# Performance work log

Hardware: AMD Instinct MI355X
Metric: run time of the kernel (lower is better)

The kernel has to match this reference:

```python
import jax, jax.numpy as jnp
import numpy as np

SA_LAMBDA = 1.0
IC_LAMBDA = 1.0
EPS = 1e-12  # torch F.normalize eps


def setup_inputs() -> dict:
    key = jax.random.key(0)
    k1, k2, k3, k4 = jax.random.split(key, 4)
    TF = jax.random.normal(k1, (16, 512, 32, 32), dtype=jnp.float32)
    SF = jax.random.normal(k2, (16, 512, 32, 32), dtype=jnp.float32)
    t_out = jax.random.normal(k3, (16, 21, 128, 128), dtype=jnp.float32)
    s_out = jax.random.normal(k4, (16, 21, 128, 128), dtype=jnp.float32)
    return {"TF": TF, "SF": SF, "t_out": t_out, "s_out": s_out}


def _l2_normalize_last(A):
    # matches torch.nn.functional.normalize(x, dim=2): x / max(||x||, eps)
    n = jnp.linalg.norm(A, axis=-1, keepdims=True)
    return A / jnp.maximum(n, EPS)


def _channel_weighted_spatial_gram(F4):
    # Algebraic fusion of einsum('bij,bki->bijk') + einsum('bijk,bi->bjk'):
    # ATT[b,m,n] = sum_c F[b,c,m] * F[b,c,n] * Fc[b,c]
    b, c, h, w = F4.shape
    Fc = jnp.sum(jnp.abs(F4), axis=(2, 3))          # [b, c]
    Fm = F4.reshape(b, c, h * w)                     # [b, c, M]
    A = jnp.einsum('bcm,bc,bcn->bmn', Fm, Fc, Fm)    # [b, M, M]
    return _l2_normalize_last(A)


def _normalized_channel_gram(L):
    # ICC[b,i,j] = sum_m L[b,i,m] * L[b,j,m], then L2-normalize along last dim
    G = jnp.einsum('bim,bjm->bij', L, L)
    return _l2_normalize_last(G)


def reference(TF, SF, t_out, s_out):
    b, c, h, w = TF.shape
    M = h * w
    ATT_T = _channel_weighted_spatial_gram(TF)
    ATT_S = _channel_weighted_spatial_gram(SF)
    diff = ATT_S - ATT_T
    SA_loss = SA_LAMBDA * jnp.sum(diff * diff) / (b * M ** 2)

    bb, cc, hh, ww = s_out.shape
    s_logit = s_out.reshape(bb, cc, hh * ww)
    t_logit = t_out.reshape(bb, cc, hh * ww)
    G_diff = _normalized_channel_gram(s_logit) - _normalized_channel_gram(t_logit)
    ic_loss = IC_LAMBDA * jnp.sum(G_diff * G_diff) / (cc * bb)

    return (s_out, ic_loss, SA_loss)
```

## Files before the change

kernel.cpp:

```cpp
#include <hip/hip_runtime.h>
#include <hip/hip_bf16.h>
#include <cstdint>
#include <cstddef>

typedef __bf16 bf16x8 __attribute__((ext_vector_type(8)));
typedef float f32x4 __attribute__((ext_vector_type(4)));

__device__ __forceinline__ void gload_lds16(const void* g, void* l) {
  __builtin_amdgcn_global_load_lds((const __attribute__((address_space(1))) void*)g,
                                   (__attribute__((address_space(3))) void*)l, 16, 0, 0);
}

__device__ __forceinline__ unsigned short f2bf(float x) {
  return __builtin_bit_cast(unsigned short, __float2bfloat16(x));
}

__global__ void __launch_bounds__(256) prep_kernel(const float* __restrict__ TF,
                                                   const float* __restrict__ SF,
                                                   __hip_bfloat16* __restrict__ Wt,
                                                   __hip_bfloat16* __restrict__ Ws) {
  __shared__ __hip_bfloat16 Xs[16 * 1040];
  __shared__ float scale[16];
  int id = blockIdx.x;
  int t = id >> 9, b = (id >> 5) & 15, cb = id & 31;
  const float* Xg = (t ? SF : TF) + ((size_t)b * 512 + (size_t)cb * 16) * 1024;
  __hip_bfloat16* W = (t ? Ws : Wt) + (size_t)b * 524288 + cb * 16;
  int tid = threadIdx.x;
  int ch = tid >> 4, seg = tid & 15;
  const float* rowp = Xg + (size_t)ch * 1024 + seg * 64;
  float s = 0.f;
#pragma unroll
  for (int i = 0; i < 16; ++i) {
    float4 v = *reinterpret_cast<const float4*>(rowp + i * 4);
    s += fabsf(v.x) + fabsf(v.y) + fabsf(v.z) + fabsf(v.w);
    ushort4 hv;
    hv.x = f2bf(v.x); hv.y = f2bf(v.y);
    hv.z = f2bf(v.z); hv.w = f2bf(v.w);
    *reinterpret_cast<ushort4*>(&Xs[ch * 1040 + seg * 64 + i * 4]) = hv;
  }
  s += __shfl_xor(s, 1); s += __shfl_xor(s, 2);
  s += __shfl_xor(s, 4); s += __shfl_xor(s, 8);
  if (seg == 0) scale[ch] = sqrtf(s);
  __syncthreads();
  float sc[16];
#pragma unroll
  for (int c = 0; c < 16; ++c) sc[c] = scale[c];
#pragma unroll
  for (int j = 0; j < 4; ++j) {
    int m = j * 256 + tid;
    union { unsigned short h[16]; uint4 u[2]; } pk;
#pragma unroll
    for (int c = 0; c < 16; ++c)
      pk.h[c] = f2bf(__bfloat162float(Xs[c * 1040 + m]) * sc[c]);
    uint4* dst = reinterpret_cast<uint4*>(W + (size_t)m * 512);
    dst[0] = pk.u[0];
    dst[1] = pk.u[1];
  }
}

__global__ void __launch_bounds__(256, 4) syrk_fused_kernel(
    const __hip_bfloat16* __restrict__ Wt, const __hip_bfloat16* __restrict__ Ws,
    float* __restrict__ nT, float* __restrict__ nS, float* __restrict__ cross) {
  __shared__ __hip_bfloat16 As2[2][128 * 32];
  __shared__ __hip_bfloat16 Bs2[2][64 * 32];
  int bid = blockIdx.x;
  int j = (bid & 7) * 144 + (bid >> 3);
  int b = j / 72, r72 = j % 72;
  int p = r72 >> 1, h = r72 & 1;
  int bx = p, tm = 0;
  while (bx >= 8 - tm) { bx -= 8 - tm; ++tm; }
  int tn = tm + bx;
  bool diag = (tm == tn);
  const __hip_bfloat16* WTb = Wt + (size_t)b * 524288;
  const __hip_bfloat16* WSb = Ws + (size_t)b * 524288;
  const __hip_bfloat16* At = WTb + (size_t)tm * 65536;
  const __hip_bfloat16* Asrc = WSb + (size_t)tm * 65536;
  const __hip_bfloat16* Btg = WTb + (size_t)(tn * 128 + h * 64) * 512;
  const __hip_bfloat16* Bsg = WSb + (size_t)(tn * 128 + h * 64) * 512;

  const int tid = threadIdx.x;
  const int lane = tid & 63, wv = tid >> 6;
  const int wr = wv >> 1, wc = wv & 1;
  const int g = lane >> 4, c0 = lane & 15;
  const int kc = (g ^ ((c0 >> 1) & 3)) * 8;

  f32x4 accT[4][2], accS[4][2];
#pragma unroll
  for (int mi = 0; mi < 4; ++mi)
#pragma unroll
    for (int ni = 0; ni < 2; ++ni) {
      accT[mi][ni] = (f32x4){0.f, 0.f, 0.f, 0.f};
      accS[mi][ni] = (f32x4){0.f, 0.f, 0.f, 0.f};
    }

  auto stage = [&](int s, int buf) {
    int kt = (s & 15) * 32;
    const __hip_bfloat16* Ab = (s < 16) ? At : Asrc;
#pragma unroll
    for (int i = 0; i < 2; ++i) {
      int ci = i * 256 + tid;
      int row = ci >> 2, slot = ci & 3;
      int gs = slot ^ ((row >> 1) & 3);
      gload_lds16(Ab + (size_t)row * 512 + kt + gs * 8, &As2[buf][(i * 256 + wv * 64) * 8]);
    }
    if (!diag) {
      const __hip_bfloat16* Bb = (s < 16) ? Btg : Bsg;
      int row = tid >> 2, slot = tid & 3;
      int gs = slot ^ ((row >> 1) & 3);
      gload_lds16(Bb + (size_t)row * 512 + kt + gs * 8, &Bs2[buf][(wv * 64) * 8]);
    }
  };

  stage(0, 0);
  __syncthreads();

  for (int s = 0; s < 32; ++s) {
    int cur = s & 1;
    if (s < 31) stage(s + 1, cur ^ 1);
    const __hip_bfloat16* Asb = As2[cur];
    const __hip_bfloat16* Bsb = diag ? (As2[cur] + h * 64 * 32) : Bs2[cur];
    bf16x8 a[4], bb[2];
#pragma unroll
    for (int mi = 0; mi < 4; ++mi)
      a[mi] = *reinterpret_cast<const bf16x8*>(Asb + (wr * 64 + mi * 16 + c0) * 32 + kc);
#pragma unroll
    for (int ni = 0; ni < 2; ++ni)
      bb[ni] = *reinterpret_cast<const bf16x8*>(Bsb + (wc * 32 + ni * 16 + c0) * 32 + kc);
    if (s < 16) {
#pragma unroll
      for (int mi = 0; mi < 4; ++mi)
#pragma unroll
        for (int ni = 0; ni < 2; ++ni)
          accT[mi][ni] = __builtin_amdgcn_mfma_f32_16x16x32_bf16(a[mi], bb[ni], accT[mi][ni], 0, 0, 0);
    } else {
#pragma unroll
      for (int mi = 0; mi < 4; ++mi)
#pragma unroll
        for (int ni = 0; ni < 2; ++ni)
          accS[mi][ni] = __builtin_amdgcn_mfma_f32_16x16x32_bf16(a[mi], bb[ni], accS[mi][ni], 0, 0, 0);
    }
    __syncthreads();
  }

  float* pT = nT + (size_t)b * 1024;
  float* pS = nS + (size_t)b * 1024;
  float* pC = cross + (size_t)b * 1024;
#pragma unroll
  for (int mi = 0; mi < 4; ++mi)
#pragma unroll
    for (int r = 0; r < 4; ++r) {
      float sT = 0.f, sS = 0.f, sC = 0.f;
#pragma unroll
      for (int ni = 0; ni < 2; ++ni) {
        float tv = accT[mi][ni][r], sv = accS[mi][ni][r];
        sT += tv * tv; sS += sv * sv; sC += tv * sv;
      }
#pragma unroll
      for (int msk = 1; msk < 16; msk <<= 1) {
        sT += __shfl_xor(sT, msk); sS += __shfl_xor(sS, msk); sC += __shfl_xor(sC, msk);
      }
      if (c0 == 0) {
        int m = tm * 128 + wr * 64 + mi * 16 + g * 4 + r;
        atomicAdd(pT + m, sT); atomicAdd(pS + m, sS); atomicAdd(pC + m, sC);
      }
    }
  if (!diag) {
#pragma unroll
    for (int ni = 0; ni < 2; ++ni) {
      float sT = 0.f, sS = 0.f, sC = 0.f;
#pragma unroll
      for (int mi = 0; mi < 4; ++mi)
#pragma unroll
        for (int r = 0; r < 4; ++r) {
          float tv = accT[mi][ni][r], sv = accS[mi][ni][r];
          sT += tv * tv; sS += sv * sv; sC += tv * sv;
        }
      sT += __shfl_xor(sT, 16); sS += __shfl_xor(sS, 16); sC += __shfl_xor(sC, 16);
      sT += __shfl_xor(sT, 32); sS += __shfl_xor(sS, 32); sC += __shfl_xor(sC, 32);
      if (g == 0) {
        int n = tn * 128 + h * 64 + wc * 32 + ni * 16 + c0;
        atomicAdd(pT + n, sT); atomicAdd(pS + n, sS); atomicAdd(pC + n, sC);
      }
    }
  }
}

__global__ void __launch_bounds__(256) icgram2_kernel(const float* __restrict__ t_out,
                                                      const float* __restrict__ s_out,
                                                      float* __restrict__ G,
                                                      float* __restrict__ outcpy) {
  __shared__ float lds[22 * 516];
  int chunk = blockIdx.x;
  int z = blockIdx.y;
  int t = z >> 4, bb = z & 15;
  const float* L = (t ? s_out : t_out) + (size_t)bb * 344064 + (size_t)chunk * 512;
  float* O = outcpy + (size_t)bb * 344064 + (size_t)chunk * 512;
  int tid = threadIdx.x;
  for (int idx = tid; idx < 22 * 128; idx += 256) {
    int r = idx >> 7, c = idx & 127;
    float4 v;
    if (r < 21) {
      v = *reinterpret_cast<const float4*>(L + (size_t)r * 16384 + c * 4);
      if (t) *reinterpret_cast<float4*>(O + (size_t)r * 16384 + c * 4) = v;
    } else { v.x = 0.f; v.y = 0.f; v.z = 0.f; v.w = 0.f; }
    *reinterpret_cast<float4*>(&lds[r * 516 + c * 4]) = v;
  }
  __syncthreads();
  int ms = tid & 3;
  for (int pb = tid >> 2; pb < 66; pb += 64) {
    int pp = pb, gi = 0;
    while (pp >= 11 - gi) { pp -= 11 - gi; gi++; }
    int gj = gi + pp;
    const float* ri0 = &lds[(2 * gi) * 516 + ms * 128];
    const float* ri1 = ri0 + 516;
    const float* rj0 = &lds[(2 * gj) * 516 + ms * 128];
    const float* rj1 = rj0 + 516;
    float a00 = 0.f, a01 = 0.f, a10 = 0.f, a11 = 0.f;
#pragma unroll
    for (int mi = 0; mi < 32; ++mi) {
      float4 va0 = *reinterpret_cast<const float4*>(ri0 + mi * 4);
      float4 va1 = *reinterpret_cast<const float4*>(ri1 + mi * 4);
      float4 vb0 = *reinterpret_cast<const float4*>(rj0 + mi * 4);
      float4 vb1 = *reinterpret_cast<const float4*>(rj1 + mi * 4);
      a00 += va0.x * vb0.x + va0.y * vb0.y + va0.z * vb0.z + va0.w * vb0.w;
      a01 += va0.x * vb1.x + va0.y * vb1.y + va0.z * vb1.z + va0.w * vb1.w;
      a10 += va1.x * vb0.x + va1.y * vb0.y + va1.z * vb0.z + va1.w * vb0.w;
      a11 += va1.x * vb1.x + va1.y * vb1.y + va1.z * vb1.z + va1.w * vb1.w;
    }
    a00 += __shfl_xor(a00, 1); a00 += __shfl_xor(a00, 2);
    a01 += __shfl_xor(a01, 1); a01 += __shfl_xor(a01, 2);
    a10 += __shfl_xor(a10, 1); a10 += __shfl_xor(a10, 2);
    a11 += __shfl_xor(a11, 1); a11 += __shfl_xor(a11, 2);
    if (ms == 0) {
      float* Gz = G + (size_t)z * 441;
      int i0 = 2 * gi, i1 = i0 + 1, j0 = 2 * gj, j1 = j0 + 1;
      atomicAdd(&Gz[i0 * 21 + j0], a00);
      if (j1 < 21) atomicAdd(&Gz[i0 * 21 + j1], a01);
      if (i1 < 21 && gi != gj) atomicAdd(&Gz[i1 * 21 + j0], a10);
      if (i1 < 21 && j1 < 21) atomicAdd(&Gz[i1 * 21 + j1], a11);
    }
  }
}

__global__ void finalize_kernel(const float* __restrict__ G, const float* __restrict__ nT,
                                const float* __restrict__ nS, const float* __restrict__ cross,
                                float* __restrict__ out2) {
  __shared__ float red[16];
  int tid = threadIdx.x;
  float sa = 0.f;
#pragma unroll
  for (int it = 0; it < 4; ++it) {
    int i4 = it * 1024 + tid;
    float4 a = reinterpret_cast<const float4*>(nT)[i4];
    float4 s4 = reinterpret_cast<const float4*>(nS)[i4];
    float4 c4 = reinterpret_cast<const float4*>(cross)[i4];
#pragma unroll
    for (int k = 0; k < 4; ++k) {
      float a1 = (&a.x)[k], s1 = (&s4.x)[k], c1 = (&c4.x)[k];
      float NT = fmaxf(sqrtf(a1), 1e-12f), NS = fmaxf(sqrtf(s1), 1e-12f);
      sa += a1 / (NT * NT) + s1 / (NS * NS) - 2.f * c1 / (NT * NS);
    }
  }
  float ic = 0.f;
  if (tid < 336) {
    int b = tid / 21, i = tid % 21;
    const float* gt = G + (size_t)b * 441;
    const float* gs = G + (size_t)(16 + b) * 441;
    float nt = 0.f, ns = 0.f;
    for (int j = 0; j < 21; ++j) {
      int idx2 = (i <= j) ? i * 21 + j : j * 21 + i;
      float vt = gt[idx2], vs = gs[idx2];
      nt += vt * vt; ns += vs * vs;
    }
    float rt = 1.f / fmaxf(sqrtf(nt), 1e-12f);
    float rs = 1.f / fmaxf(sqrtf(ns), 1e-12f);
    for (int j = 0; j < 21; ++j) {
      int idx2 = (i <= j) ? i * 21 + j : j * 21 + i;
      float d = gs[idx2] * rs - gt[idx2] * rt;
      ic += d * d;
    }
  }
  int lane = tid & 63, wv = tid >> 6;
#pragma unroll
  for (int m = 32; m; m >>= 1) { sa += __shfl_xor(sa, m); ic += __shfl_xor(ic, m); }
  if (lane == 0) red[wv] = sa;
  __syncthreads();
  if (tid == 0) { float s = 0.f; for (int w = 0; w < 16; ++w) s += red[w]; out2[1] = s * (1.0f / 16777216.0f); }
  __syncthreads();
  if (lane == 0) red[wv] = ic;
  __syncthreads();
  if (tid == 0) { float s = 0.f; for (int w = 0; w < 16; ++w) s += red[w]; out2[0] = s * (1.0f / 336.0f); }
}

extern "C" void kernel_launch(void* const* d_in, const int* in_sizes, int n_in,
                              void* d_out, int out_size, void* d_ws, size_t ws_size,
                              hipStream_t stream) {
  const float* TF = (const float*)d_in[0];
  const float* SF = (const float*)d_in[1];
  const float* t_out = (const float*)d_in[2];
  const float* s_out = (const float*)d_in[3];
  float* out = (float*)d_out;
  char* ws = (char*)d_ws;

  float* nT = (float*)(ws + 0);
  float* nS = (float*)(ws + 65536);
  float* cross = (float*)(ws + 131072);
  float* G = (float*)(ws + 196608);
  __hip_bfloat16* Wt = (__hip_bfloat16*)(ws + 262144);
  __hip_bfloat16* Ws = (__hip_bfloat16*)(ws + 262144 + 16777216);

  (void)hipMemsetAsync(ws, 0, 253056, stream);

  prep_kernel<<<1024, 256, 0, stream>>>(TF, SF, Wt, Ws);
  syrk_fused_kernel<<<1152, 256, 0, stream>>>(Wt, Ws, nT, nS, cross);
  icgram2_kernel<<<dim3(32, 32), 256, 0, stream>>>(t_out, s_out, G, out);
  finalize_kernel<<<1, 1024, 0, stream>>>(G, nT, nS, cross, out + 5505024);
}
```

Before: 150.0 us.

## Split prep into Fc and transpose kernels, enlarge SYRK tiles to 128x128

The single prep kernel becomes two: one computes sqrt of per-channel abs sums, and a tiled 64x64 LDS transpose writes the scaled bf16 W matrix with coalesced 16-byte stores. The SYRK kernel now uses 512 threads with full 128x128 tiles and K-steps of 64, so each block computes a whole tile pair instead of half-tiles, and the block count is halved. It uses explicit vmcnt waits and raw barriers so the next stage's loads overlap compute. Diagonal tiles now load B redundantly, and the extra kernel launch and a second read of TF/SF add cost.

```diff
diff --git a/kernel.cpp b/kernel.cpp
--- a/kernel.cpp
+++ b/kernel.cpp
@@ -10,148 +10,167 @@
   __builtin_amdgcn_global_load_lds((const __attribute__((address_space(1))) void*)g,
                                    (__attribute__((address_space(3))) void*)l, 16, 0, 0);
 }
-
 __device__ __forceinline__ unsigned short f2bf(float x) {
   return __builtin_bit_cast(unsigned short, __float2bfloat16(x));
 }
-
-__global__ void __launch_bounds__(256) prep_kernel(const float* __restrict__ TF,
-                                                   const float* __restrict__ SF,
-                                                   __hip_bfloat16* __restrict__ Wt,
-                                                   __hip_bfloat16* __restrict__ Ws) {
-  __shared__ __hip_bfloat16 Xs[16 * 1040];
-  __shared__ float scale[16];
-  int id = blockIdx.x;
-  int t = id >> 9, b = (id >> 5) & 15, cb = id & 31;
-  const float* Xg = (t ? SF : TF) + ((size_t)b * 512 + (size_t)cb * 16) * 1024;
-  __hip_bfloat16* W = (t ? Ws : Wt) + (size_t)b * 524288 + cb * 16;
+#define S_BARRIER asm volatile("s_barrier" ::: "memory")
+#define WAIT_VM(N) asm volatile("s_waitcnt vmcnt(" #N ")" ::: "memory")
+
+__global__ void fc_kernel(const float* __restrict__ TF, const float* __restrict__ SF,
+                          float* __restrict__ sqrtFc) {
+  int wv = threadIdx.x >> 6, lane = threadIdx.x & 63;
+  int row = blockIdx.x * 4 + wv;
+  const float* X = (row < 8192) ? TF : SF;
+  const float* p = X + (size_t)(row & 8191) * 1024;
+  float s = 0.f;
+#pragma unroll
+  for (int it = 0; it < 4; ++it) {
+    float4 v = *reinterpret_cast<const float4*>(p + (size_t)(it * 64 + lane) * 4);
+    s += fabsf(v.x) + fabsf(v.y) + fabsf(v.z) + fabsf(v.w);
+  }
+#pragma unroll
+  for (int m = 32; m; m >>= 1) s += __shfl_xor(s, m);
+  if (lane == 0) sqrtFc[row] = sqrtf(s);
+}
+
+__global__ void __launch_bounds__(256) wprep2_kernel(const float* __restrict__ TF,
+                                                     const float* __restrict__ SF,
+                                                     const float* __restrict__ sqrtFc,
+                                                     __hip_bfloat16* __restrict__ Wt,
+                                                     __hip_bfloat16* __restrict__ Ws) {
+  __shared__ float lds[64][65];
+  __shared__ float scale[64];
+  int z = blockIdx.z;
+  int t = z >> 4, b = z & 15;
+  int m0 = blockIdx.x * 64, c0 = blockIdx.y * 64;
+  const float* Xg = (t ? SF : TF) + (size_t)b * 524288;
+  __hip_bfloat16* Wg = (t ? Ws : Wt) + (size_t)b * 524288;
   int tid = threadIdx.x;
-  int ch = tid >> 4, seg = tid & 15;
-  const float* rowp = Xg + (size_t)ch * 1024 + seg * 64;
-  float s = 0.f;
-#pragma unroll
-  for (int i = 0; i < 16; ++i) {
-    float4 v = *reinterpret_cast<const float4*>(rowp + i * 4);
-    s += fabsf(v.x) + fabsf(v.y) + fabsf(v.z) + fabsf(v.w);
-    ushort4 hv;
-    hv.x = f2bf(v.x); hv.y = f2bf(v.y);
-    hv.z = f2bf(v.z); hv.w = f2bf(v.w);
-    *reinterpret_cast<ushort4*>(&Xs[ch * 1040 + seg * 64 + i * 4]) = hv;
-  }
-  s += __shfl_xor(s, 1); s += __shfl_xor(s, 2);
-  s += __shfl_xor(s, 4); s += __shfl_xor(s, 8);
-  if (seg == 0) scale[ch] = sqrtf(s);
-  __syncthreads();
-  float sc[16];
-#pragma unroll
-  for (int c = 0; c < 16; ++c) sc[c] = scale[c];
-#pragma unroll
-  for (int j = 0; j < 4; ++j) {
-    int m = j * 256 + tid;
-    union { unsigned short h[16]; uint4 u[2]; } pk;
-#pragma unroll
-    for (int c = 0; c < 16; ++c)
-      pk.h[c] = f2bf(__bfloat162float(Xs[c * 1040 + m]) * sc[c]);
-    uint4* dst = reinterpret_cast<uint4*>(W + (size_t)m * 512);
-    dst[0] = pk.u[0];
-    dst[1] = pk.u[1];
-  }
-}
-
-__global__ void __launch_bounds__(256, 4) syrk_fused_kernel(
+  if (tid < 64) scale[tid] = sqrtFc[t * 8192 + b * 512 + c0 + tid];
+#pragma unroll
+  for (int i = 0; i < 4; ++i) {
+    int v = i * 256 + tid;
+    int r = v >> 4, q = v & 15;
+    *reinterpret_cast<float4*>(&lds[r][q * 4]) =
+        *reinterpret_cast<const float4*>(Xg + (size_t)(c0 + r) * 1024 + m0 + q * 4);
+  }
+  __syncthreads();
+#pragma unroll
+  for (int jj = 0; jj < 2; ++jj) {
+    int m = jj * 32 + (tid >> 3), oct = tid & 7;
+    union { unsigned short h[8]; uint4 u; } pk;
+#pragma unroll
+    for (int k = 0; k < 8; ++k) {
+      int c = oct * 8 + k;
+      pk.h[k] = f2bf(lds[c][m] * scale[c]);
+    }
+    *reinterpret_cast<uint4*>(Wg + (size_t)(m0 + m) * 512 + c0 + oct * 8) = pk.u;
+  }
+}
+
+__global__ void __launch_bounds__(512, 4) syrk_fused_kernel(
     const __hip_bfloat16* __restrict__ Wt, const __hip_bfloat16* __restrict__ Ws,
     float* __restrict__ nT, float* __restrict__ nS, float* __restrict__ cross) {
-  __shared__ __hip_bfloat16 As2[2][128 * 32];
-  __shared__ __hip_bfloat16 Bs2[2][64 * 32];
+  __shared__ __hip_bfloat16 AL[2][128 * 64];
+  __shared__ __hip_bfloat16 BL[2][128 * 64];
   int bid = blockIdx.x;
-  int j = (bid & 7) * 144 + (bid >> 3);
-  int b = j / 72, r72 = j % 72;
-  int p = r72 >> 1, h = r72 & 1;
-  int bx = p, tm = 0;
+  int j = (bid & 7) * 72 + (bid >> 3);
+  int b = j / 36, pair = j % 36;
+  int bx = pair, tm = 0;
   while (bx >= 8 - tm) { bx -= 8 - tm; ++tm; }
   int tn = tm + bx;
   bool diag = (tm == tn);
   const __hip_bfloat16* WTb = Wt + (size_t)b * 524288;
   const __hip_bfloat16* WSb = Ws + (size_t)b * 524288;
-  const __hip_bfloat16* At = WTb + (size_t)tm * 65536;
-  const __hip_bfloat16* Asrc = WSb + (size_t)tm * 65536;
-  const __hip_bfloat16* Btg = WTb + (size_t)(tn * 128 + h * 64) * 512;
-  const __hip_bfloat16* Bsg = WSb + (size_t)(tn * 128 + h * 64) * 512;
+  const __hip_bfloat16* ATp = WTb + (size_t)tm * 65536;
+  const __hip_bfloat16* ASp = WSb + (size_t)tm * 65536;
+  const __hip_bfloat16* BTp = WTb + (size_t)tn * 65536;
+  const __hip_bfloat16* BSp = WSb + (size_t)tn * 65536;
 
   const int tid = threadIdx.x;
   const int lane = tid & 63, wv = tid >> 6;
   const int wr = wv >> 1, wc = wv & 1;
-  const int g = lane >> 4, c0 = lane & 15;
-  const int kc = (g ^ ((c0 >> 1) & 3)) * 8;
-
-  f32x4 accT[4][2], accS[4][2];
-#pragma unroll
-  for (int mi = 0; mi < 4; ++mi)
-#pragma unroll
-    for (int ni = 0; ni < 2; ++ni) {
+  const int g = lane >> 4, c0 = lane & 15, cx = c0 & 7;
+
+  int offs[2], dst[2];
+#pragma unroll
+  for (int i = 0; i < 2; ++i) {
+    int ci = i * 512 + tid;
+    int row = ci >> 3, slot = ci & 7;
+    offs[i] = row * 512 + (slot ^ (row & 7)) * 8;
+    dst[i] = (i * 512 + wv * 64) * 8;
+  }
+
+  f32x4 accT[2][4], accS[2][4];
+#pragma unroll
+  for (int mi = 0; mi < 2; ++mi)
+#pragma unroll
+    for (int ni = 0; ni < 4; ++ni) {
       accT[mi][ni] = (f32x4){0.f, 0.f, 0.f, 0.f};
       accS[mi][ni] = (f32x4){0.f, 0.f, 0.f, 0.f};
     }
 
   auto stage = [&](int s, int buf) {
-    int kt = (s & 15) * 32;
-    const __hip_bfloat16* Ab = (s < 16) ? At : Asrc;
+    int kt = (s & 7) * 64;
+    const __hip_bfloat16* Ab = (s < 8) ? ATp : ASp;
+    const __hip_bfloat16* Bb = (s < 8) ? BTp : BSp;
 #pragma unroll
     for (int i = 0; i < 2; ++i) {
-      int ci = i * 256 + tid;
-      int row = ci >> 2, slot = ci & 3;
-      int gs = slot ^ ((row >> 1) & 3);
-      gload_lds16(Ab + (size_t)row * 512 + kt + gs * 8, &As2[buf][(i * 256 + wv * 64) * 8]);
-    }
-    if (!diag) {
-      const __hip_bfloat16* Bb = (s < 16) ? Btg : Bsg;
-      int row = tid >> 2, slot = tid & 3;
-      int gs = slot ^ ((row >> 1) & 3);
-      gload_lds16(Bb + (size_t)row * 512 + kt + gs * 8, &Bs2[buf][(wv * 64) * 8]);
+      gload_lds16(Ab + offs[i] + kt, &AL[buf][dst[i]]);
+      gload_lds16(Bb + offs[i] + kt, &BL[buf][dst[i]]);
     }
   };
 
   stage(0, 0);
-  __syncthreads();
-
-  for (int s = 0; s < 32; ++s) {
-    int cur = s & 1;
-    if (s < 31) stage(s + 1, cur ^ 1);
-    const __hip_bfloat16* Asb = As2[cur];
-    const __hip_bfloat16* Bsb = diag ? (As2[cur] + h * 64 * 32) : Bs2[cur];
-    bf16x8 a[4], bb[2];
-#pragma unroll
-    for (int mi = 0; mi < 4; ++mi)
-      a[mi] = *reinterpret_cast<const bf16x8*>(Asb + (wr * 64 + mi * 16 + c0) * 32 + kc);
-#pragma unroll
-    for (int ni = 0; ni < 2; ++ni)
-      bb[ni] = *reinterpret_cast<const bf16x8*>(Bsb + (wc * 32 + ni * 16 + c0) * 32 + kc);
-    if (s < 16) {
-#pragma unroll
-      for (int mi = 0; mi < 4; ++mi)
-#pragma unroll
-        for (int ni = 0; ni < 2; ++ni)
-          accT[mi][ni] = __builtin_amdgcn_mfma_f32_16x16x32_bf16(a[mi], bb[ni], accT[mi][ni], 0, 0, 0);
+#pragma unroll
+  for (int s = 0; s < 16; ++s) {
+    int buf = s & 1;
+    if (s < 15) {
+      stage(s + 1, buf ^ 1);
+      WAIT_VM(4);
     } else {
-#pragma unroll
-      for (int mi = 0; mi < 4; ++mi)
-#pragma unroll
-        for (int ni = 0; ni < 2; ++ni)
-          accS[mi][ni] = __builtin_amdgcn_mfma_f32_16x16x32_bf16(a[mi], bb[ni], accS[mi][ni], 0, 0, 0);
-    }
-    __syncthreads();
+      WAIT_VM(0);
+    }
+    S_BARRIER;
+    const __hip_bfloat16* Ab = AL[buf];
+    const __hip_bfloat16* Bb = BL[buf];
+#pragma unroll
+    for (int kk = 0; kk < 2; ++kk) {
+      int ck = ((kk * 4 + g) ^ cx) * 8;
+      bf16x8 av[2], bv[4];
+#pragma unroll
+      for (int mi = 0; mi < 2; ++mi)
+        av[mi] = *reinterpret_cast<const bf16x8*>(Ab + (wr * 32 + mi * 16 + c0) * 64 + ck);
+#pragma unroll
+      for (int ni = 0; ni < 4; ++ni)
+        bv[ni] = *reinterpret_cast<const bf16x8*>(Bb + (wc * 64 + ni * 16 + c0) * 64 + ck);
+      if (s < 8) {
+#pragma unroll
+        for (int mi = 0; mi < 2; ++mi)
+#pragma unroll
+          for (int ni = 0; ni < 4; ++ni)
+            accT[mi][ni] = __builtin_amdgcn_mfma_f32_16x16x32_bf16(av[mi], bv[ni], accT[mi][ni], 0, 0, 0);
+      } else {
+#pragma unroll
+        for (int mi = 0; mi < 2; ++mi)
+#pragma unroll
+          for (int ni = 0; ni < 4; ++ni)
+            accS[mi][ni] = __builtin_amdgcn_mfma_f32_16x16x32_bf16(av[mi], bv[ni], accS[mi][ni], 0, 0, 0);
+      }
+    }
+    if (s < 15) S_BARRIER;
   }
 
   float* pT = nT + (size_t)b * 1024;
   float* pS = nS + (size_t)b * 1024;
   float* pC = cross + (size_t)b * 1024;
 #pragma unroll
-  for (int mi = 0; mi < 4; ++mi)
+  for (int mi = 0; mi < 2; ++mi)
 #pragma unroll
     for (int r = 0; r < 4; ++r) {
       float sT = 0.f, sS = 0.f, sC = 0.f;
 #pragma unroll
-      for (int ni = 0; ni < 2; ++ni) {
+      for (int ni = 0; ni < 4; ++ni) {
         float tv = accT[mi][ni][r], sv = accS[mi][ni][r];
         sT += tv * tv; sS += sv * sv; sC += tv * sv;
       }
@@ -160,16 +179,16 @@
         sT += __shfl_xor(sT, msk); sS += __shfl_xor(sS, msk); sC += __shfl_xor(sC, msk);
       }
       if (c0 == 0) {
-        int m = tm * 128 + wr * 64 + mi * 16 + g * 4 + r;
+        int m = tm * 128 + wr * 32 + mi * 16 + g * 4 + r;
         atomicAdd(pT + m, sT); atomicAdd(pS + m, sS); atomicAdd(pC + m, sC);
       }
     }
   if (!diag) {
 #pragma unroll
-    for (int ni = 0; ni < 2; ++ni) {
+    for (int ni = 0; ni < 4; ++ni) {
       float sT = 0.f, sS = 0.f, sC = 0.f;
 #pragma unroll
-      for (int mi = 0; mi < 4; ++mi)
+      for (int mi = 0; mi < 2; ++mi)
 #pragma unroll
         for (int r = 0; r < 4; ++r) {
           float tv = accT[mi][ni][r], sv = accS[mi][ni][r];
@@ -178,7 +197,7 @@
       sT += __shfl_xor(sT, 16); sS += __shfl_xor(sS, 16); sC += __shfl_xor(sC, 16);
       sT += __shfl_xor(sT, 32); sS += __shfl_xor(sS, 32); sC += __shfl_xor(sC, 32);
       if (g == 0) {
-        int n = tn * 128 + h * 64 + wc * 32 + ni * 16 + c0;
+        int n = tn * 128 + wc * 64 + ni * 16 + c0;
         atomicAdd(pT + n, sT); atomicAdd(pS + n, sS); atomicAdd(pC + n, sC);
       }
     }
@@ -306,13 +325,15 @@
   float* nS = (float*)(ws + 65536);
   float* cross = (float*)(ws + 131072);
   float* G = (float*)(ws + 196608);
-  __hip_bfloat16* Wt = (__hip_bfloat16*)(ws + 262144);
-  __hip_bfloat16* Ws = (__hip_bfloat16*)(ws + 262144 + 16777216);
+  float* sqrtFc = (float*)(ws + 253184);
+  __hip_bfloat16* Wt = (__hip_bfloat16*)(ws + 318720);
+  __hip_bfloat16* Ws = (__hip_bfloat16*)(ws + 318720 + 16777216);
 
   (void)hipMemsetAsync(ws, 0, 253056, stream);
 
-  prep_kernel<<<1024, 256, 0, stream>>>(TF, SF, Wt, Ws);
-  syrk_fused_kernel<<<1152, 256, 0, stream>>>(Wt, Ws, nT, nS, cross);
+  fc_kernel<<<4096, 256, 0, stream>>>(TF, SF, sqrtFc);
+  wprep2_kernel<<<dim3(16, 8, 32), 256, 0, stream>>>(TF, SF, sqrtFc, Wt, Ws);
+  syrk_fused_kernel<<<576, 512, 0, stream>>>(Wt, Ws, nT, nS, cross);
   icgram2_kernel<<<dim3(32, 32), 256, 0, stream>>>(t_out, s_out, G, out);
   finalize_kernel<<<1, 1024, 0, stream>>>(G, nT, nS, cross, out + 5505024);
 }
```

New measurement: 130.5 us. -13.0%, faster.
